# Performance work log

Hardware: AMD Instinct MI355X
Metric: run time of the kernel (lower is better)

## Reference

```python
import jax, jax.numpy as jnp
import numpy as np

D = 1024
H = 16
DH = D // H


def setup_inputs() -> dict:
    key = jax.random.key(0)
    ks = jax.random.split(key, 7)
    s = 0.02
    return {
        "z": jax.random.normal(ks[0], (8, 1024, D), dtype=jnp.float32),
        "ln_w": jnp.ones((D,), dtype=jnp.float32),
        "ln_b": jnp.zeros((D,), dtype=jnp.float32),
        "W_qkv": jax.random.normal(ks[1], (D, 3 * D), dtype=jnp.float32) * s,
        "b_qkv": jnp.zeros((3 * D,), dtype=jnp.float32),
        "W_proj": jax.random.normal(ks[2], (D, D), dtype=jnp.float32) * s,
        "b_proj": jnp.zeros((D,), dtype=jnp.float32),
    }


def reference(z, ln_w, ln_b, W_qkv, b_qkv, W_proj, b_proj):
    b, n, d = z.shape
    # Pre-LN
    mu = jnp.mean(z, axis=-1, keepdims=True)
    var = jnp.var(z, axis=-1, keepdims=True)
    zn = (z - mu) / jnp.sqrt(var + 1e-5) * ln_w + ln_b
    # QKV projection: [b, n, 3, H, DH]
    qkv = (zn @ W_qkv + b_qkv).reshape(b, n, 3, H, DH)
    q = qkv[:, :, 0].transpose(0, 2, 1, 3)  # [b, H, n, DH]
    k = qkv[:, :, 1].transpose(0, 2, 1, 3)
    v = qkv[:, :, 2].transpose(0, 2, 1, 3)
    scale = 1.0 / jnp.sqrt(jnp.asarray(DH, dtype=z.dtype))
    scores = jnp.einsum("bhqd,bhkd->bhqk", q, k) * scale
    attn = jax.nn.softmax(scores, axis=-1)
    msa = jnp.einsum("bhqk,bhkd->bhqd", attn, v)  # [b, H, n, DH]
    msa_cat = msa.transpose(0, 2, 1, 3).reshape(b, n, d)
    out = msa_cat @ W_proj + b_proj
    return z + out
```

## Files before the change

kernel.cpp:

```cpp
#include <hip/hip_runtime.h>
#include <stdint.h>

typedef unsigned short u16;
typedef uint8_t u8;
typedef __bf16 bf16x8 __attribute__((ext_vector_type(8)));
typedef float f32x4 __attribute__((ext_vector_type(4)));
typedef int i32x8 __attribute__((ext_vector_type(8)));

#define D_MODEL 1024
#define NHEADS  16
#define DHEAD   64
#define BATCH   8
#define SEQ     1024
#define MTOT    (BATCH*SEQ)

#define GPTR(p) ((const __attribute__((address_space(1))) void*)(p))
#define LPTR(p) ((__attribute__((address_space(3))) void*)(p))

#if defined(__HIP_DEVICE_COMPILE__)
  #define MFMA_FP8_16x16x128(a, b, c) \
      __builtin_amdgcn_mfma_scale_f32_16x16x128_f8f6f4((a), (b), (c), 0, 0, 0, 127, 0, 127)
  #define CVT_PK_FP8(a, b, old, w) __builtin_amdgcn_cvt_pk_fp8_f32((a), (b), (old), (w))
#else
  #define MFMA_FP8_16x16x128(a, b, c) (c)
  #define CVT_PK_FP8(a, b, old, w) (0)
#endif

__device__ __forceinline__ u16 f2bf(float f) {
    union { float f; uint32_t u; } v; v.f = f;
    uint32_t u = v.u;
    u += 0x7fffu + ((u >> 16) & 1u);
    return (u16)(u >> 16);
}

__device__ __forceinline__ uint32_t pklo(int i1, int i0) {
    return __builtin_amdgcn_perm((uint32_t)i1, (uint32_t)i0, 0x05040100u);
}

__global__ __launch_bounds__(256) void ln_kernel(
    const float* __restrict__ z, const float* __restrict__ w,
    const float* __restrict__ b, uint32_t* __restrict__ znf)
{
    const int row = blockIdx.x;
    const int t = threadIdx.x;
    const float4 v = reinterpret_cast<const float4*>(z + (size_t)row * D_MODEL)[t];
    float s  = v.x + v.y + v.z + v.w;
    float s2 = v.x*v.x + v.y*v.y + v.z*v.z + v.w*v.w;
    #pragma unroll
    for (int off = 32; off; off >>= 1) {
        s  += __shfl_down(s,  off, 64);
        s2 += __shfl_down(s2, off, 64);
    }
    __shared__ float red[8];
    const int wave = t >> 6, lane = t & 63;
    if (lane == 0) { red[wave] = s; red[wave + 4] = s2; }
    __syncthreads();
    if (t == 0) {
        float ts  = red[0] + red[1] + red[2] + red[3];
        float ts2 = red[4] + red[5] + red[6] + red[7];
        float mu  = ts * (1.0f / D_MODEL);
        float var = ts2 * (1.0f / D_MODEL) - mu * mu;
        red[0] = mu; red[1] = rsqrtf(var + 1e-5f);
    }
    __syncthreads();
    const float mu = red[0], rstd = red[1];
    const float4 wv = reinterpret_cast<const float4*>(w)[t];
    const float4 bv = reinterpret_cast<const float4*>(b)[t];
    const float x0 = (v.x - mu) * rstd * wv.x + bv.x;
    const float x1 = (v.y - mu) * rstd * wv.y + bv.y;
    const float x2 = (v.z - mu) * rstd * wv.z + bv.z;
    const float x3 = (v.w - mu) * rstd * wv.w + bv.w;
    int pk = CVT_PK_FP8(x0, x1, 0, false);
    pk = CVT_PK_FP8(x2, x3, pk, true);
    znf[(size_t)row * (D_MODEL / 4) + t] = (uint32_t)pk;
}

__global__ __launch_bounds__(256) void transpose_cast(
    const float* __restrict__ in, u16* __restrict__ out, int R, int C)
{
    __shared__ u16 tile[32][33];
    const int c0 = blockIdx.x * 32, r0 = blockIdx.y * 32;
    const int tx = threadIdx.x & 31, ty = threadIdx.x >> 5;
    #pragma unroll
    for (int i = 0; i < 4; ++i)
        tile[ty + i*8][tx] = f2bf(in[(size_t)(r0 + ty + i*8) * C + c0 + tx]);
    __syncthreads();
    #pragma unroll
    for (int i = 0; i < 4; ++i)
        out[(size_t)(c0 + ty + i*8) * R + r0 + tx] = tile[tx][ty + i*8];
}

__global__ __launch_bounds__(256) void transpose_cast_fp8(
    const float* __restrict__ in, u8* __restrict__ out, int R, int C)
{
    __shared__ u8 tile[32][36];
    const int c0 = blockIdx.x * 32, r0 = blockIdx.y * 32;
    const int tx = threadIdx.x & 31, ty = threadIdx.x >> 5;
    #pragma unroll
    for (int i = 0; i < 4; ++i) {
        const float f = in[(size_t)(r0 + ty + i*8) * C + c0 + tx];
        tile[ty + i*8][tx] = (u8)(CVT_PK_FP8(f, 0.f, 0, false) & 0xFF);
    }
    __syncthreads();
    #pragma unroll
    for (int i = 0; i < 4; ++i)
        out[(size_t)(c0 + ty + i*8) * R + r0 + tx] = tile[tx][ty + i*8];
}

__global__ __launch_bounds__(256) void transpose_v(
    const u16* __restrict__ in, u16* __restrict__ out)
{
    __shared__ u16 tile[64][65];
    const int bh = blockIdx.y;
    const int t0 = blockIdx.x * 64;
    const int tid = threadIdx.x;
    const u16* src = in + ((size_t)bh * SEQ + t0) * DHEAD;
    #pragma unroll
    for (int i = 0; i < 4; ++i) {
        const int row = (tid >> 4) + i * 16;
        const int c4  = (tid & 15) * 4;
        *reinterpret_cast<ushort4*>(&tile[row][c4]) =
            *reinterpret_cast<const ushort4*>(&src[(size_t)row * DHEAD + c4]);
    }
    __syncthreads();
    u16* dst = out + (size_t)bh * DHEAD * SEQ + t0;
    #pragma unroll
    for (int i = 0; i < 4; ++i) {
        const int dh = (tid >> 4) + i * 16;
        const int tt = (tid & 15) * 4;
        ushort4 o;
        o.x = tile[tt+0][dh]; o.y = tile[tt+1][dh];
        o.z = tile[tt+2][dh]; o.w = tile[tt+3][dh];
        *reinterpret_cast<ushort4*>(&dst[(size_t)dh * SEQ + tt]) = o;
    }
}

#define QSCALE 0.180336880f

__global__ __launch_bounds__(256, 2) void gemm_qkv(
    const u8* __restrict__ A, const u8* __restrict__ Bt,
    const float* __restrict__ bias,
    u16* __restrict__ q, u16* __restrict__ k, u16* __restrict__ v)
{
    __shared__ u8 As[128 * 128];
    __shared__ u8 Bs[128 * 128];
    const int tid = threadIdx.x;
    const int wave = tid >> 6, lane = tid & 63;
    const int lm = lane & 15, g = lane >> 4;
    const int wm = (wave >> 1) * 64, wn = (wave & 1) * 64;
    const int m0 = blockIdx.y * 128, n0 = blockIdx.x * 128;
    const int srow = tid >> 3;
    const int sseg = tid & 7;
    const int sgcol = (sseg ^ (srow & 7)) * 16;
    const int xl = lm & 7;
    const int ca0 = ((2 * g) ^ xl) * 16;
    const int ca1 = ((2 * g + 1) ^ xl) * 16;
    f32x4 acc[4][4] = {};
    for (int k0 = 0; k0 < D_MODEL; k0 += 128) {
        #pragma unroll
        for (int c = 0; c < 4; ++c) {
            const int r = srow + c * 32;
            __builtin_amdgcn_global_load_lds(
                GPTR(&A[(size_t)(m0 + r) * D_MODEL + k0 + sgcol]),
                LPTR(&As[r * 128 + sseg * 16]), 16, 0, 0);
            __builtin_amdgcn_global_load_lds(
                GPTR(&Bt[(size_t)(n0 + r) * D_MODEL + k0 + sgcol]),
                LPTR(&Bs[r * 128 + sseg * 16]), 16, 0, 0);
        }
        __syncthreads();
        i32x8 af[4], bfr[4];
        #pragma unroll
        for (int i = 0; i < 4; ++i) {
            const uint4 alo = *reinterpret_cast<const uint4*>(&As[(wm + i*16 + lm) * 128 + ca0]);
            const uint4 ahi = *reinterpret_cast<const uint4*>(&As[(wm + i*16 + lm) * 128 + ca1]);
            af[i][0] = alo.x; af[i][1] = alo.y; af[i][2] = alo.z; af[i][3] = alo.w;
            af[i][4] = ahi.x; af[i][5] = ahi.y; af[i][6] = ahi.z; af[i][7] = ahi.w;
            const uint4 blo = *reinterpret_cast<const uint4*>(&Bs[(wn + i*16 + lm) * 128 + ca0]);
            const uint4 bhi = *reinterpret_cast<const uint4*>(&Bs[(wn + i*16 + lm) * 128 + ca1]);
            bfr[i][0] = blo.x; bfr[i][1] = blo.y; bfr[i][2] = blo.z; bfr[i][3] = blo.w;
            bfr[i][4] = bhi.x; bfr[i][5] = bhi.y; bfr[i][6] = bhi.z; bfr[i][7] = bhi.w;
        }
        #pragma unroll
        for (int i = 0; i < 4; ++i)
            #pragma unroll
            for (int j = 0; j < 4; ++j)
                acc[i][j] = MFMA_FP8_16x16x128(bfr[j], af[i], acc[i][j]);
        __syncthreads();
    }
    const int colbase = n0 + wn;
    const int sel = colbase >> 10;
    const int h = (colbase & 1023) >> 6;
    u16* dst = (sel == 0) ? q : (sel == 1) ? k : v;
    const float scl = (sel == 0) ? QSCALE : 1.0f;
    #pragma unroll
    for (int j = 0; j < 4; ++j) {
        const int dh0 = j * 16 + 4 * g;
        const float4 bv4 = *reinterpret_cast<const float4*>(&bias[colbase + dh0]);
        #pragma unroll
        for (int i = 0; i < 4; ++i) {
            const int m = m0 + wm + i * 16 + lm;
            const int b = m >> 10, t = m & 1023;
            ushort4 o;
            o.x = f2bf((acc[i][j][0] + bv4.x) * scl);
            o.y = f2bf((acc[i][j][1] + bv4.y) * scl);
            o.z = f2bf((acc[i][j][2] + bv4.z) * scl);
            o.w = f2bf((acc[i][j][3] + bv4.w) * scl);
            *reinterpret_cast<ushort4*>(
                &dst[(((size_t)(b * NHEADS + h)) * SEQ + t) * DHEAD + dh0]) = o;
        }
    }
}

__global__ __launch_bounds__(256, 2) void gemm_proj(
    const u16* __restrict__ A, const u16* __restrict__ Bt,
    const float* __restrict__ bias, const float* __restrict__ z,
    float* __restrict__ out)
{
    __shared__ u16 As[128 * 64];
    __shared__ u16 Bs[128 * 64];
    const int tid = threadIdx.x;
    const int wave = tid >> 6, lane = tid & 63;
    const int lm = lane & 15, g = lane >> 4;
    const int wm = (wave >> 1) * 64, wn = (wave & 1) * 64;
    const int m0 = blockIdx.y * 128, n0 = blockIdx.x * 128;
    const int srow = tid >> 3;
    const int sseg = tid & 7;
    const int sgcol = (sseg ^ (srow & 7)) * 8;
    const int xl = lm & 7;
    f32x4 acc[4][4] = {};
    for (int k0 = 0; k0 < D_MODEL; k0 += 64) {
        #pragma unroll
        for (int c = 0; c < 4; ++c) {
            const int r = srow + c * 32;
            __builtin_amdgcn_global_load_lds(
                GPTR(&A[(size_t)(m0 + r) * D_MODEL + k0 + sgcol]),
                LPTR(&As[r * 64 + sseg * 8]), 16, 0, 0);
            __builtin_amdgcn_global_load_lds(
                GPTR(&Bt[(size_t)(n0 + r) * D_MODEL + k0 + sgcol]),
                LPTR(&Bs[r * 64 + sseg * 8]), 16, 0, 0);
        }
        __syncthreads();
        #pragma unroll
        for (int ko = 0; ko < 2; ++ko) {
            const int ca = ((ko * 4 + g) ^ xl) * 8;
            bf16x8 af[4], bfr[4];
            #pragma unroll
            for (int i = 0; i < 4; ++i) {
                af[i]  = *reinterpret_cast<const bf16x8*>(&As[(wm + i*16 + lm) * 64 + ca]);
                bfr[i] = *reinterpret_cast<const bf16x8*>(&Bs[(wn + i*16 + lm) * 64 + ca]);
            }
            #pragma unroll
            for (int i = 0; i < 4; ++i)
                #pragma unroll
                for (int j = 0; j < 4; ++j)
                    acc[i][j] = __builtin_amdgcn_mfma_f32_16x16x32_bf16(
                        bfr[j], af[i], acc[i][j], 0, 0, 0);
        }
        __syncthreads();
    }
    #pragma unroll
    for (int j = 0; j < 4; ++j) {
        const int col0 = n0 + wn + j * 16 + 4 * g;
        const float4 bv4 = *reinterpret_cast<const float4*>(&bias[col0]);
        #pragma unroll
        for (int i = 0; i < 4; ++i) {
            const int m = m0 + wm + i * 16 + lm;
            const size_t idx = (size_t)m * D_MODEL + col0;
            const float4 zv = *reinterpret_cast<const float4*>(&z[idx]);
            float4 ov;
            ov.x = zv.x + acc[i][j][0] + bv4.x;
            ov.y = zv.y + acc[i][j][1] + bv4.y;
            ov.z = zv.z + acc[i][j][2] + bv4.z;
            ov.w = zv.w + acc[i][j][3] + bv4.w;
            *reinterpret_cast<float4*>(&out[idx]) = ov;
        }
    }
}

#define KLD 68

__global__ __launch_bounds__(256, 4) void attn_kernel(
    const u16* __restrict__ Q, const u16* __restrict__ K,
    const u16* __restrict__ Vt, u16* __restrict__ msa)
{
    __shared__ u16 Ks[64 * KLD];
    __shared__ u16 Vs[64 * KLD];
    const int tid = threadIdx.x, wave = tid >> 6, lane = tid & 63;
    const int lm = lane & 15, g = lane >> 4;
    const int bi = blockIdx.x;
    const int bh = bi & 127;
    const int q0 = (bi >> 7) * 128;
    const int b = bh >> 4, h = bh & 15;
    const size_t headBase = (size_t)bh * SEQ * DHEAD;
    const u16* Qh = Q + headBase;
    const u16* Kh = K + headBase;
    const u16* Vh = Vt + headBase;

    const int srow = tid >> 3, sseg = tid & 7;
    const int aA = 16 * (sseg >> 2) + 4 * (sseg & 3);

    const uint4 onesu = {0x3F803F80u, 0x3F803F80u, 0x3F803F80u, 0x3F803F80u};
    const bf16x8 ONES = __builtin_bit_cast(bf16x8, onesu);

    bf16x8 qf[2][2];
    #pragma unroll
    for (int s = 0; s < 2; ++s) {
        const u16* qrow = Qh + (size_t)(q0 + s * 64 + wave * 16 + lm) * DHEAD;
        qf[s][0] = *reinterpret_cast<const bf16x8*>(qrow + g * 8);
        qf[s][1] = *reinterpret_cast<const bf16x8*>(qrow + 32 + g * 8);
    }

    f32x4 o[2][4] = {};
    f32x4 lacc[2] = {};

    for (int j0 = 0; j0 < SEQ; j0 += 64) {
        #pragma unroll
        for (int s2 = 0; s2 < 2; ++s2) {
            const int row = srow + 32 * s2;
            *reinterpret_cast<uint4*>(&Ks[row * KLD + sseg * 8]) =
                *reinterpret_cast<const uint4*>(&Kh[(size_t)(j0 + row) * DHEAD + sseg * 8]);
            const u16* vrow = Vh + (size_t)row * SEQ + j0;
            const uint2 va = *reinterpret_cast<const uint2*>(vrow + aA);
            const uint2 vb = *reinterpret_cast<const uint2*>(vrow + 32 + aA);
            uint4 wv; wv.x = va.x; wv.y = va.y; wv.z = vb.x; wv.w = vb.y;
            *reinterpret_cast<uint4*>(&Vs[row * KLD + sseg * 8]) = wv;
        }
        __syncthreads();

        bf16x8 kf0[4], kf1[4];
        #pragma unroll
        for (int ni = 0; ni < 4; ++ni) {
            kf0[ni] = *reinterpret_cast<const bf16x8*>(&Ks[(ni*16 + lm) * KLD + g * 8]);
            kf1[ni] = *reinterpret_cast<const bf16x8*>(&Ks[(ni*16 + lm) * KLD + 32 + g * 8]);
        }

        bf16x8 pfr[2][2];
        #pragma unroll
        for (int s = 0; s < 2; ++s) {
            f32x4 st[4];
            #pragma unroll
            for (int ni = 0; ni < 4; ++ni) {
                f32x4 zero = {};
                st[ni] = __builtin_amdgcn_mfma_f32_16x16x32_bf16(kf0[ni], qf[s][0], zero, 0, 0, 0);
                st[ni] = __builtin_amdgcn_mfma_f32_16x16x32_bf16(kf1[ni], qf[s][1], st[ni], 0, 0, 0);
            }
            int ip[4][4];
            #pragma unroll
            for (int ni = 0; ni < 4; ++ni)
                #pragma unroll
                for (int r = 0; r < 4; ++r)
                    ip[ni][r] = (int)__builtin_fmaf(st[ni][r], 128.0f, 16250.5f);
            #pragma unroll
            for (int c = 0; c < 2; ++c) {
                uint4 u;
                u.x = pklo(ip[c][1],   ip[c][0]);
                u.y = pklo(ip[c][3],   ip[c][2]);
                u.z = pklo(ip[c+2][1], ip[c+2][0]);
                u.w = pklo(ip[c+2][3], ip[c+2][2]);
                pfr[s][c] = __builtin_bit_cast(bf16x8, u);
            }
            lacc[s] = __builtin_amdgcn_mfma_f32_16x16x32_bf16(ONES, pfr[s][0], lacc[s], 0, 0, 0);
            lacc[s] = __builtin_amdgcn_mfma_f32_16x16x32_bf16(ONES, pfr[s][1], lacc[s], 0, 0, 0);
        }

        #pragma unroll
        for (int mt = 0; mt < 4; ++mt) {
            bf16x8 vf0 = *reinterpret_cast<const bf16x8*>(&Vs[(mt*16 + lm) * KLD + g * 8]);
            bf16x8 vf1 = *reinterpret_cast<const bf16x8*>(&Vs[(mt*16 + lm) * KLD + 32 + g * 8]);
            #pragma unroll
            for (int s = 0; s < 2; ++s) {
                o[s][mt] = __builtin_amdgcn_mfma_f32_16x16x32_bf16(vf0, pfr[s][0], o[s][mt], 0, 0, 0);
                o[s][mt] = __builtin_amdgcn_mfma_f32_16x16x32_bf16(vf1, pfr[s][1], o[s][mt], 0, 0, 0);
            }
        }
        __syncthreads();
    }

    #pragma unroll
    for (int s = 0; s < 2; ++s) {
        const float inv = 1.0f / lacc[s][0];
        const int t = q0 + s * 64 + wave * 16 + lm;
        const size_t base = ((size_t)b * SEQ + t) * D_MODEL + h * DHEAD;
        #pragma unroll
        for (int mt = 0; mt < 4; ++mt) {
            const int d0 = mt * 16 + 4 * g;
            ushort4 pk;
            pk.x = f2bf(o[s][mt][0] * inv);
            pk.y = f2bf(o[s][mt][1] * inv);
            pk.z = f2bf(o[s][mt][2] * inv);
            pk.w = f2bf(o[s][mt][3] * inv);
            *reinterpret_cast<ushort4*>(&msa[base + d0]) = pk;
        }
    }
}

extern "C" void kernel_launch(void* const* d_in, const int* in_sizes, int n_in,
                              void* d_out, int out_size, void* d_ws, size_t ws_size,
                              hipStream_t stream) {
    const float* z      = (const float*)d_in[0];
    const float* ln_w   = (const float*)d_in[1];
    const float* ln_b   = (const float*)d_in[2];
    const float* W_qkv  = (const float*)d_in[3];
    const float* b_qkv  = (const float*)d_in[4];
    const float* W_proj = (const float*)d_in[5];
    const float* b_proj = (const float*)d_in[6];
    float* out = (float*)d_out;

    u8* ws = (u8*)d_ws;
    u8*  znf    = ws;
    u8*  wqkvTf = znf + (size_t)MTOT * D_MODEL;
    u16* wprojT = (u16*)(wqkvTf + (size_t)3 * D_MODEL * D_MODEL);
    u16* q      = wprojT + (size_t)D_MODEL * D_MODEL;
    u16* k      = q + (size_t)MTOT * D_MODEL;
    u16* vtmp   = k + (size_t)MTOT * D_MODEL;
    u16* vT     = vtmp + (size_t)MTOT * D_MODEL;
    u16* msa    = vtmp;

    ln_kernel<<<MTOT, 256, 0, stream>>>(z, ln_w, ln_b, (uint32_t*)znf);
    transpose_cast_fp8<<<dim3(3 * D_MODEL / 32, D_MODEL / 32), 256, 0, stream>>>(
        W_qkv, wqkvTf, D_MODEL, 3 * D_MODEL);
    transpose_cast<<<dim3(D_MODEL / 32, D_MODEL / 32), 256, 0, stream>>>(
        W_proj, wprojT, D_MODEL, D_MODEL);
    gemm_qkv<<<dim3(3 * D_MODEL / 128, MTOT / 128), 256, 0, stream>>>(
        znf, wqkvTf, b_qkv, q, k, vtmp);
    transpose_v<<<dim3(SEQ / 64, BATCH * NHEADS), 256, 0, stream>>>(vtmp, vT);
    attn_kernel<<<BATCH * NHEADS * (SEQ / 128), 256, 0, stream>>>(q, k, vT, msa);
    gemm_proj<<<dim3(D_MODEL / 128, MTOT / 128), 256, 0, stream>>>(
        msa, wprojT, b_proj, z, out);
}
```

Baseline: 225.6 us.

## Fuse V transpose into QKV GEMM, merge weight prep, run proj GEMM in FP8

The QKV GEMM now swaps MFMA operand order for V-column blocks so it can write V already transposed, which removes the separate transpose_v kernel and its round trip through memory. The two weight transpose/cast kernels become one launch, and W_proj is now cast to FP8. The attention kernel writes its output as FP8, and the projection GEMM switches from bf16 to the FP8 128-wide-K MFMA path, halving its operand bytes. The cost is lower precision in the projection GEMM, and the transposed V stores are narrow and strided.

Measured after the change: 206.4 us. 1.09x faster.

```diff
diff --git a/kernel.cpp b/kernel.cpp
--- a/kernel.cpp
+++ b/kernel.cpp
@@ -75,26 +75,16 @@
     znf[(size_t)row * (D_MODEL / 4) + t] = (uint32_t)pk;
 }
 
-__global__ __launch_bounds__(256) void transpose_cast(
-    const float* __restrict__ in, u16* __restrict__ out, int R, int C)
-{
-    __shared__ u16 tile[32][33];
-    const int c0 = blockIdx.x * 32, r0 = blockIdx.y * 32;
-    const int tx = threadIdx.x & 31, ty = threadIdx.x >> 5;
-    #pragma unroll
-    for (int i = 0; i < 4; ++i)
-        tile[ty + i*8][tx] = f2bf(in[(size_t)(r0 + ty + i*8) * C + c0 + tx]);
-    __syncthreads();
-    #pragma unroll
-    for (int i = 0; i < 4; ++i)
-        out[(size_t)(c0 + ty + i*8) * R + r0 + tx] = tile[tx][ty + i*8];
-}
-
-__global__ __launch_bounds__(256) void transpose_cast_fp8(
-    const float* __restrict__ in, u8* __restrict__ out, int R, int C)
+__global__ __launch_bounds__(256) void prep_weights(
+    const float* __restrict__ Wqkv, const float* __restrict__ Wproj,
+    u8* __restrict__ outQkv, u8* __restrict__ outProj)
 {
     __shared__ u8 tile[32][36];
-    const int c0 = blockIdx.x * 32, r0 = blockIdx.y * 32;
+    const int bx = blockIdx.x;
+    const float* in; u8* out; int C;
+    if (bx < 96) { in = Wqkv;  out = outQkv;  C = 3072; }
+    else         { in = Wproj; out = outProj; C = 1024; }
+    const int c0 = (bx < 96 ? bx : bx - 96) * 32, r0 = blockIdx.y * 32;
     const int tx = threadIdx.x & 31, ty = threadIdx.x >> 5;
     #pragma unroll
     for (int i = 0; i < 4; ++i) {
@@ -104,35 +94,7 @@
     __syncthreads();
     #pragma unroll
     for (int i = 0; i < 4; ++i)
-        out[(size_t)(c0 + ty + i*8) * R + r0 + tx] = tile[tx][ty + i*8];
-}
-
-__global__ __launch_bounds__(256) void transpose_v(
-    const u16* __restrict__ in, u16* __restrict__ out)
-{
-    __shared__ u16 tile[64][65];
-    const int bh = blockIdx.y;
-    const int t0 = blockIdx.x * 64;
-    const int tid = threadIdx.x;
-    const u16* src = in + ((size_t)bh * SEQ + t0) * DHEAD;
-    #pragma unroll
-    for (int i = 0; i < 4; ++i) {
-        const int row = (tid >> 4) + i * 16;
-        const int c4  = (tid & 15) * 4;
-        *reinterpret_cast<ushort4*>(&tile[row][c4]) =
-            *reinterpret_cast<const ushort4*>(&src[(size_t)row * DHEAD + c4]);
-    }
-    __syncthreads();
-    u16* dst = out + (size_t)bh * DHEAD * SEQ + t0;
-    #pragma unroll
-    for (int i = 0; i < 4; ++i) {
-        const int dh = (tid >> 4) + i * 16;
-        const int tt = (tid & 15) * 4;
-        ushort4 o;
-        o.x = tile[tt+0][dh]; o.y = tile[tt+1][dh];
-        o.z = tile[tt+2][dh]; o.w = tile[tt+3][dh];
-        *reinterpret_cast<ushort4*>(&dst[(size_t)dh * SEQ + tt]) = o;
-    }
+        out[(size_t)(c0 + ty + i*8) * D_MODEL + r0 + tx] = tile[tx][ty + i*8];
 }
 
 #define QSCALE 0.180336880f
@@ -140,7 +102,110 @@
 __global__ __launch_bounds__(256, 2) void gemm_qkv(
     const u8* __restrict__ A, const u8* __restrict__ Bt,
     const float* __restrict__ bias,
-    u16* __restrict__ q, u16* __restrict__ k, u16* __restrict__ v)
+    u16* __restrict__ q, u16* __restrict__ k, u16* __restrict__ vT)
+{
+    __shared__ u8 As[128 * 128];
+    __shared__ u8 Bs[128 * 128];
+    const int tid = threadIdx.x;
+    const int wave = tid >> 6, lane = tid & 63;
+    const int lm = lane & 15, g = lane >> 4;
+    const int wm = (wave >> 1) * 64, wn = (wave & 1) * 64;
+    const int m0 = blockIdx.y * 128, n0 = blockIdx.x * 128;
+    const int srow = tid >> 3;
+    const int sseg = tid & 7;
+    const int sgcol = (sseg ^ (srow & 7)) * 16;
+    const int xl = lm & 7;
+    const int ca0 = ((2 * g) ^ xl) * 16;
+    const int ca1 = ((2 * g + 1) ^ xl) * 16;
+    const bool isV = (blockIdx.x >= 16);
+    f32x4 acc[4][4] = {};
+    for (int k0 = 0; k0 < D_MODEL; k0 += 128) {
+        #pragma unroll
+        for (int c = 0; c < 4; ++c) {
+            const int r = srow + c * 32;
+            __builtin_amdgcn_global_load_lds(
+                GPTR(&A[(size_t)(m0 + r) * D_MODEL + k0 + sgcol]),
+                LPTR(&As[r * 128 + sseg * 16]), 16, 0, 0);
+            __builtin_amdgcn_global_load_lds(
+                GPTR(&Bt[(size_t)(n0 + r) * D_MODEL + k0 + sgcol]),
+                LPTR(&Bs[r * 128 + sseg * 16]), 16, 0, 0);
+        }
+        __syncthreads();
+        i32x8 af[4], bfr[4];
+        #pragma unroll
+        for (int i = 0; i < 4; ++i) {
+            const uint4 alo = *reinterpret_cast<const uint4*>(&As[(wm + i*16 + lm) * 128 + ca0]);
+            const uint4 ahi = *reinterpret_cast<const uint4*>(&As[(wm + i*16 + lm) * 128 + ca1]);
+            af[i][0] = alo.x; af[i][1] = alo.y; af[i][2] = alo.z; af[i][3] = alo.w;
+            af[i][4] = ahi.x; af[i][5] = ahi.y; af[i][6] = ahi.z; af[i][7] = ahi.w;
+            const uint4 blo = *reinterpret_cast<const uint4*>(&Bs[(wn + i*16 + lm) * 128 + ca0]);
+            const uint4 bhi = *reinterpret_cast<const uint4*>(&Bs[(wn + i*16 + lm) * 128 + ca1]);
+            bfr[i][0] = blo.x; bfr[i][1] = blo.y; bfr[i][2] = blo.z; bfr[i][3] = blo.w;
+            bfr[i][4] = bhi.x; bfr[i][5] = bhi.y; bfr[i][6] = bhi.z; bfr[i][7] = bhi.w;
+        }
+        if (!isV) {
+            #pragma unroll
+            for (int i = 0; i < 4; ++i)
+                #pragma unroll
+                for (int j = 0; j < 4; ++j)
+                    acc[i][j] = MFMA_FP8_16x16x128(bfr[j], af[i], acc[i][j]);
+        } else {
+            #pragma unroll
+            for (int i = 0; i < 4; ++i)
+                #pragma unroll
+                for (int j = 0; j < 4; ++j)
+                    acc[i][j] = MFMA_FP8_16x16x128(af[i], bfr[j], acc[i][j]);
+        }
+        __syncthreads();
+    }
+    const int colbase = n0 + wn;
+    const int h = (colbase & 1023) >> 6;
+    if (!isV) {
+        const int sel = colbase >> 10;
+        u16* dst = (sel == 0) ? q : k;
+        const float scl = (sel == 0) ? QSCALE : 1.0f;
+        #pragma unroll
+        for (int j = 0; j < 4; ++j) {
+            const int dh0 = j * 16 + 4 * g;
+            const float4 bv4 = *reinterpret_cast<const float4*>(&bias[colbase + dh0]);
+            #pragma unroll
+            for (int i = 0; i < 4; ++i) {
+                const int m = m0 + wm + i * 16 + lm;
+                const int b = m >> 10, t = m & 1023;
+                ushort4 o;
+                o.x = f2bf((acc[i][j][0] + bv4.x) * scl);
+                o.y = f2bf((acc[i][j][1] + bv4.y) * scl);
+                o.z = f2bf((acc[i][j][2] + bv4.z) * scl);
+                o.w = f2bf((acc[i][j][3] + bv4.w) * scl);
+                *reinterpret_cast<ushort4*>(
+                    &dst[(((size_t)(b * NHEADS + h)) * SEQ + t) * DHEAD + dh0]) = o;
+            }
+        }
+    } else {
+        #pragma unroll
+        for (int j = 0; j < 4; ++j) {
+            const int dh = j * 16 + lm;
+            const float bv = bias[colbase + dh];
+            #pragma unroll
+            for (int i = 0; i < 4; ++i) {
+                const int t0 = m0 + wm + i * 16 + 4 * g;
+                const int b = t0 >> 10, t = t0 & 1023;
+                ushort4 o;
+                o.x = f2bf(acc[i][j][0] + bv);
+                o.y = f2bf(acc[i][j][1] + bv);
+                o.z = f2bf(acc[i][j][2] + bv);
+                o.w = f2bf(acc[i][j][3] + bv);
+                *reinterpret_cast<ushort4*>(
+                    &vT[(((size_t)(b * NHEADS + h)) * DHEAD + dh) * SEQ + t]) = o;
+            }
+        }
+    }
+}
+
+__global__ __launch_bounds__(256, 2) void gemm_proj(
+    const u8* __restrict__ A, const u8* __restrict__ Bt,
+    const float* __restrict__ bias, const float* __restrict__ z,
+    float* __restrict__ out)
 {
     __shared__ u8 As[128 * 128];
     __shared__ u8 Bs[128 * 128];
@@ -187,77 +252,6 @@
                 acc[i][j] = MFMA_FP8_16x16x128(bfr[j], af[i], acc[i][j]);
         __syncthreads();
     }
-    const int colbase = n0 + wn;
-    const int sel = colbase >> 10;
-    const int h = (colbase & 1023) >> 6;
-    u16* dst = (sel == 0) ? q : (sel == 1) ? k : v;
-    const float scl = (sel == 0) ? QSCALE : 1.0f;
-    #pragma unroll
-    for (int j = 0; j < 4; ++j) {
-        const int dh0 = j * 16 + 4 * g;
-        const float4 bv4 = *reinterpret_cast<const float4*>(&bias[colbase + dh0]);
-        #pragma unroll
-        for (int i = 0; i < 4; ++i) {
-            const int m = m0 + wm + i * 16 + lm;
-            const int b = m >> 10, t = m & 1023;
-            ushort4 o;
-            o.x = f2bf((acc[i][j][0] + bv4.x) * scl);
-            o.y = f2bf((acc[i][j][1] + bv4.y) * scl);
-            o.z = f2bf((acc[i][j][2] + bv4.z) * scl);
-            o.w = f2bf((acc[i][j][3] + bv4.w) * scl);
-            *reinterpret_cast<ushort4*>(
-                &dst[(((size_t)(b * NHEADS + h)) * SEQ + t) * DHEAD + dh0]) = o;
-        }
-    }
-}
-
-__global__ __launch_bounds__(256, 2) void gemm_proj(
-    const u16* __restrict__ A, const u16* __restrict__ Bt,
-    const float* __restrict__ bias, const float* __restrict__ z,
-    float* __restrict__ out)
-{
-    __shared__ u16 As[128 * 64];
-    __shared__ u16 Bs[128 * 64];
-    const int tid = threadIdx.x;
-    const int wave = tid >> 6, lane = tid & 63;
-    const int lm = lane & 15, g = lane >> 4;
-    const int wm = (wave >> 1) * 64, wn = (wave & 1) * 64;
-    const int m0 = blockIdx.y * 128, n0 = blockIdx.x * 128;
-    const int srow = tid >> 3;
-    const int sseg = tid & 7;
-    const int sgcol = (sseg ^ (srow & 7)) * 8;
-    const int xl = lm & 7;
-    f32x4 acc[4][4] = {};
-    for (int k0 = 0; k0 < D_MODEL; k0 += 64) {
-        #pragma unroll
-        for (int c = 0; c < 4; ++c) {
-            const int r = srow + c * 32;
-            __builtin_amdgcn_global_load_lds(
-                GPTR(&A[(size_t)(m0 + r) * D_MODEL + k0 + sgcol]),
-                LPTR(&As[r * 64 + sseg * 8]), 16, 0, 0);
-            __builtin_amdgcn_global_load_lds(
-                GPTR(&Bt[(size_t)(n0 + r) * D_MODEL + k0 + sgcol]),
-                LPTR(&Bs[r * 64 + sseg * 8]), 16, 0, 0);
-        }
-        __syncthreads();
-        #pragma unroll
-        for (int ko = 0; ko < 2; ++ko) {
-            const int ca = ((ko * 4 + g) ^ xl) * 8;
-            bf16x8 af[4], bfr[4];
-            #pragma unroll
-            for (int i = 0; i < 4; ++i) {
-                af[i]  = *reinterpret_cast<const bf16x8*>(&As[(wm + i*16 + lm) * 64 + ca]);
-                bfr[i] = *reinterpret_cast<const bf16x8*>(&Bs[(wn + i*16 + lm) * 64 + ca]);
-            }
-            #pragma unroll
-            for (int i = 0; i < 4; ++i)
-                #pragma unroll
-                for (int j = 0; j < 4; ++j)
-                    acc[i][j] = __builtin_amdgcn_mfma_f32_16x16x32_bf16(
-                        bfr[j], af[i], acc[i][j], 0, 0, 0);
-        }
-        __syncthreads();
-    }
     #pragma unroll
     for (int j = 0; j < 4; ++j) {
         const int col0 = n0 + wn + j * 16 + 4 * g;
@@ -281,7 +275,7 @@
 
 __global__ __launch_bounds__(256, 4) void attn_kernel(
     const u16* __restrict__ Q, const u16* __restrict__ K,
-    const u16* __restrict__ Vt, u16* __restrict__ msa)
+    const u16* __restrict__ Vt, u8* __restrict__ msaf)
 {
     __shared__ u16 Ks[64 * KLD];
     __shared__ u16 Vs[64 * KLD];
@@ -384,12 +378,9 @@
         #pragma unroll
         for (int mt = 0; mt < 4; ++mt) {
             const int d0 = mt * 16 + 4 * g;
-            ushort4 pk;
-            pk.x = f2bf(o[s][mt][0] * inv);
-            pk.y = f2bf(o[s][mt][1] * inv);
-            pk.z = f2bf(o[s][mt][2] * inv);
-            pk.w = f2bf(o[s][mt][3] * inv);
-            *reinterpret_cast<ushort4*>(&msa[base + d0]) = pk;
+            int pk = CVT_PK_FP8(o[s][mt][0] * inv, o[s][mt][1] * inv, 0, false);
+            pk = CVT_PK_FP8(o[s][mt][2] * inv, o[s][mt][3] * inv, pk, true);
+            *reinterpret_cast<uint32_t*>(&msaf[base + d0]) = (uint32_t)pk;
         }
     }
 }
@@ -407,24 +398,19 @@
     float* out = (float*)d_out;
 
     u8* ws = (u8*)d_ws;
-    u8*  znf    = ws;
-    u8*  wqkvTf = znf + (size_t)MTOT * D_MODEL;
-    u16* wprojT = (u16*)(wqkvTf + (size_t)3 * D_MODEL * D_MODEL);
-    u16* q      = wprojT + (size_t)D_MODEL * D_MODEL;
-    u16* k      = q + (size_t)MTOT * D_MODEL;
-    u16* vtmp   = k + (size_t)MTOT * D_MODEL;
-    u16* vT     = vtmp + (size_t)MTOT * D_MODEL;
-    u16* msa    = vtmp;
+    u8*  znf     = ws;
+    u8*  wqkvTf  = znf + (size_t)MTOT * D_MODEL;
+    u8*  wprojTf = wqkvTf + (size_t)3 * D_MODEL * D_MODEL;
+    u8*  msaf    = wprojTf + (size_t)D_MODEL * D_MODEL;
+    u16* q       = (u16*)(msaf + (size_t)MTOT * D_MODEL);
+    u16* k       = q + (size_t)MTOT * D_MODEL;
+    u16* vT      = k + (size_t)MTOT * D_MODEL;
 
     ln_kernel<<<MTOT, 256, 0, stream>>>(z, ln_w, ln_b, (uint32_t*)znf);
-    transpose_cast_fp8<<<dim3(3 * D_MODEL / 32, D_MODEL / 32), 256, 0, stream>>>(
-        W_qkv, wqkvTf, D_MODEL, 3 * D_MODEL);
-    transpose_cast<<<dim3(D_MODEL / 32, D_MODEL / 32), 256, 0, stream>>>(
-        W_proj, wprojT, D_MODEL, D_MODEL);
+    prep_weights<<<dim3(128, 32), 256, 0, stream>>>(W_qkv, W_proj, wqkvTf, wprojTf);
     gemm_qkv<<<dim3(3 * D_MODEL / 128, MTOT / 128), 256, 0, stream>>>(
-        znf, wqkvTf, b_qkv, q, k, vtmp);
-    transpose_v<<<dim3(SEQ / 64, BATCH * NHEADS), 256, 0, stream>>>(vtmp, vT);
-    attn_kernel<<<BATCH * NHEADS * (SEQ / 128), 256, 0, stream>>>(q, k, vT, msa);
+        znf, wqkvTf, b_qkv, q, k, vT);
+    attn_kernel<<<BATCH * NHEADS * (SEQ / 128), 256, 0, stream>>>(q, k, vT, msaf);
     gemm_proj<<<dim3(D_MODEL / 128, MTOT / 128), 256, 0, stream>>>(
-        msa, wprojT, b_proj, z, out);
-}
+        msaf, wprojTf, b_proj, z, out);
+}
```
